# Performance work log

Measured on AMD Instinct MI355X. Metric: run time of the kernel, lower is better.

The kernel has to match this reference:

```python
import jax, jax.numpy as jnp
import numpy as np

B, N, C, H = 8, 1024, 1024, 16  # batch, seq, dim, heads
HID = 4 * C                     # mlp hidden (mlp_ratio=4.0)


def _ln(x, g, b, eps=1e-5):
    m = x.mean(-1, keepdims=True)
    v = ((x - m) ** 2).mean(-1, keepdims=True)
    return (x - m) / jnp.sqrt(v + eps) * g + b


def setup_inputs() -> dict:
    key = jax.random.key(0)
    ks = jax.random.split(key, 8)
    s = 0.02  # init scale
    f32 = jnp.float32
    return {
        "x": jax.random.normal(ks[0], (B, N, C), f32),
        "g1": jnp.ones((C,), f32), "b1": jnp.zeros((C,), f32),
        "Wq": jax.random.normal(ks[1], (C, C), f32) * s, "bq": jnp.zeros((C,), f32),
        "Wk": jax.random.normal(ks[2], (C, C), f32) * s, "bk": jnp.zeros((C,), f32),
        "Wv": jax.random.normal(ks[3], (C, C), f32) * s, "bv": jnp.zeros((C,), f32),
        "Wp": jax.random.normal(ks[4], (C, C), f32) * s, "bp": jnp.zeros((C,), f32),
        "g2": jnp.ones((C,), f32), "b2": jnp.zeros((C,), f32),
        "W1": jax.random.normal(ks[5], (C, HID), f32) * s, "c1": jnp.zeros((HID,), f32),
        "W2": jax.random.normal(ks[6], (HID, C), f32) * s, "c2": jnp.zeros((C,), f32),
    }


def reference(x, g1, b1, Wq, bq, Wk, bk, Wv, bv, Wp, bp, g2, b2, W1, c1, W2, c2):
    hd = C // H
    scale = hd ** -0.5
    # --- pre-norm self-attention ---
    h = _ln(x, g1, b1)
    # NOTE: faithful to source: direct reshape (B,N,C)->(B,H,N,hd), NOT the
    # standard reshape(B,N,H,hd).transpose -- the original code reshapes the
    # flat N*C block into H contiguous chunks of N*hd.
    q = (h @ Wq + bq).reshape(B, H, -1, hd)
    k = (h @ Wk + bk).reshape(B, H, -1, hd)
    v = (h @ Wv + bv).reshape(B, H, -1, hd)
    attn = jax.nn.softmax(jnp.einsum('bhnd,bhmd->bhnm', q, k) * scale, axis=-1)
    o = jnp.einsum('bhnm,bhmd->bhnd', attn, v)
    o = jnp.swapaxes(o, 1, 2).reshape(B, -1, C)  # (B,N,C)
    x = x + (o @ Wp + bp)
    # --- MLP block ---
    h2 = _ln(x, g2, b2)
    m = jax.nn.gelu(h2 @ W1 + c1, approximate=False) @ W2 + c2
    return x + m
```

## Files before the change

### kernel.cpp

```cpp
#include <hip/hip_runtime.h>
#include <hip/hip_bf16.h>
#include <math.h>

typedef __bf16 bf16_t;
typedef __bf16 bf16x4 __attribute__((ext_vector_type(4)));
typedef __bf16 bf16x8 __attribute__((ext_vector_type(8)));
typedef float  f32x4  __attribute__((ext_vector_type(4)));

typedef __attribute__((address_space(1))) const void GVoid;
typedef __attribute__((address_space(3))) void LVoid;

__device__ __forceinline__ void gld16(const void* g, void* l) {
    __builtin_amdgcn_global_load_lds((GVoid*)g, (LVoid*)l, 16, 0, 0);
}

__device__ __forceinline__ float gelu_exact(float v) {
    return 0.5f * v * (1.0f + erff(v * 0.7071067811865475f));
}

__global__ __launch_bounds__(256) void transpose_f32_bf16(
    const float* __restrict__ in, bf16_t* __restrict__ out,
    int R, int C, size_t inBatch, size_t outBatch)
{
    __shared__ bf16_t tile[64][65];
    const float* src = in  + (size_t)blockIdx.z * inBatch;
    bf16_t*      dst = out + (size_t)blockIdx.z * outBatch;
    const int r0 = blockIdx.y * 64, c0 = blockIdx.x * 64;
    const int t = threadIdx.x, tc = t & 63, tr = t >> 6;
#pragma unroll
    for (int i = 0; i < 16; ++i) {
        int r = tr + i * 4;
        tile[r][tc] = (bf16_t)src[(size_t)(r0 + r) * C + c0 + tc];
    }
    __syncthreads();
#pragma unroll
    for (int i = 0; i < 16; ++i) {
        int r = tr + i * 4;
        dst[(size_t)(c0 + r) * R + r0 + tc] = tile[tc][r];
    }
}

__global__ __launch_bounds__(256) void transpose_bf16(
    const bf16_t* __restrict__ in, bf16_t* __restrict__ out,
    int R, int C, size_t inBatch, size_t outBatch)
{
    __shared__ __align__(16) bf16_t tile[64][65];
    const bf16_t* src = in  + (size_t)blockIdx.z * inBatch;
    bf16_t*       dst = out + (size_t)blockIdx.z * outBatch;
    const int r0 = blockIdx.y * 64, c0 = blockIdx.x * 64;
    const int t = threadIdx.x, tc = t & 63, tr = t >> 6;
#pragma unroll
    for (int i = 0; i < 16; ++i) {
        int r = tr + i * 4;
        tile[r][tc] = src[(size_t)(r0 + r) * C + c0 + tc];
    }
    __syncthreads();
#pragma unroll
    for (int i = 0; i < 16; ++i) {
        int r = tr + i * 4;
        dst[(size_t)(c0 + r) * R + r0 + tc] = tile[tc][r];
    }
}

__global__ __launch_bounds__(256) void ln_kernel(
    const float* __restrict__ x, const float* __restrict__ g,
    const float* __restrict__ b, bf16_t* __restrict__ out)
{
    const int row = blockIdx.x, t = threadIdx.x;
    const float4 v4 = ((const float4*)(x + (size_t)row * 1024))[t];
    float v[4] = {v4.x, v4.y, v4.z, v4.w};
    float s = v[0] + v[1] + v[2] + v[3];
    float s2 = v[0]*v[0] + v[1]*v[1] + v[2]*v[2] + v[3]*v[3];
#pragma unroll
    for (int o = 1; o < 64; o <<= 1) { s += __shfl_xor(s, o); s2 += __shfl_xor(s2, o); }
    __shared__ float red[8];
    if ((t & 63) == 0) { red[t >> 6] = s; red[4 + (t >> 6)] = s2; }
    __syncthreads();
    s  = red[0] + red[1] + red[2] + red[3];
    s2 = red[4] + red[5] + red[6] + red[7];
    const float mean = s * (1.f / 1024.f);
    const float var  = fmaxf(s2 * (1.f / 1024.f) - mean * mean, 0.f);
    const float rstd = rsqrtf(var + 1e-5f);
    const float4 g4 = ((const float4*)g)[t];
    const float4 b4 = ((const float4*)b)[t];
    bf16x4 o;
    o[0] = (bf16_t)((v[0] - mean) * rstd * g4.x + b4.x);
    o[1] = (bf16_t)((v[1] - mean) * rstd * g4.y + b4.y);
    o[2] = (bf16_t)((v[2] - mean) * rstd * g4.z + b4.z);
    o[3] = (bf16_t)((v[3] - mean) * rstd * g4.w + b4.w);
    *(bf16x4*)(out + (size_t)row * 1024 + t * 4) = o;
}

__device__ __forceinline__ bf16x8 lds_rd(const char* base, int rl, int colB) {
    return *(const bf16x8*)(base + rl * 128 + (colB ^ ((rl & 7) << 4)));
}

template <int MODE>
__global__ __launch_bounds__(512, 2) void gemm256(
    const bf16_t* __restrict__ A, const bf16_t* __restrict__ Bt,
    const float* __restrict__ b0, const float* __restrict__ b1,
    const float* __restrict__ b2, const float* resid,
    bf16_t* __restrict__ ob0, bf16_t* __restrict__ ob1,
    bf16_t* __restrict__ ob2, float* of,
    int N, int K)
{
    __shared__ __align__(16) char lds[131072];
    const int t = threadIdx.x;
    const int w = t >> 6, ln = t & 63;
    const int wm = w >> 2, wn = w & 3;
    const int l16 = ln & 15, quad = ln >> 4;
    const int m0 = blockIdx.x * 256, n0 = blockIdx.y * 256;

    const bf16_t* gA = A  + (size_t)m0 * K;
    const bf16_t* gB = Bt + (size_t)n0 * K;

    const int w1k  = w << 10;
    const int srow = t >> 3;
    const int scol = ((t & 7) ^ (srow & 7)) << 3;

    auto stage = [&](int kt, int dbuf) {
        char* aL = (char*)lds + dbuf * 32768 + w1k;
        char* bL = (char*)lds + 65536 + dbuf * 32768 + w1k;
#pragma unroll
        for (int h = 0; h < 2; ++h) {
#pragma unroll
            for (int r2 = 0; r2 < 2; ++r2) {
                const int row = h * 128 + r2 * 64 + srow;
                gld16(gA + (size_t)row * K + kt + scol, aL + h * 16384 + r2 * 8192);
                gld16(gB + (size_t)row * K + kt + scol, bL + h * 16384 + r2 * 8192);
            }
        }
    };

    f32x4 acc[8][4];
#pragma unroll
    for (int i = 0; i < 8; ++i)
#pragma unroll
        for (int j = 0; j < 4; ++j) acc[i][j] = f32x4{0.f, 0.f, 0.f, 0.f};

    const int ktiles = K >> 6;
    stage(0, 0);
    stage(64, 1);
    asm volatile("s_waitcnt vmcnt(8)" ::: "memory");
    __builtin_amdgcn_s_barrier();
    __builtin_amdgcn_sched_barrier(0);

    bf16x8 af[4][2], bfr[4][2];

    for (int kt = 0; kt < ktiles; ++kt) {
        const int b = kt & 1;
        const char* aB = (const char*)lds + b * 32768 + wm * 16384;
        const char* bB = (const char*)lds + 65536 + b * 32768 + (wn >> 1) * 16384;
        const int bR0 = (wn & 1) << 6;

#pragma unroll
        for (int i = 0; i < 4; ++i)
#pragma unroll
            for (int ks = 0; ks < 2; ++ks)
                af[i][ks] = lds_rd(aB, i * 16 + l16, ks * 64 + quad * 16);
#pragma unroll
        for (int j = 0; j < 2; ++j)
#pragma unroll
            for (int ks = 0; ks < 2; ++ks)
                bfr[j][ks] = lds_rd(bB, bR0 + j * 16 + l16, ks * 64 + quad * 16);
        __builtin_amdgcn_s_setprio(1);
#pragma unroll
        for (int i = 0; i < 4; ++i)
#pragma unroll
            for (int j = 0; j < 2; ++j)
#pragma unroll
                for (int ks = 0; ks < 2; ++ks)
                    acc[i][j] = __builtin_amdgcn_mfma_f32_16x16x32_bf16(
                        af[i][ks], bfr[j][ks], acc[i][j], 0, 0, 0);
        __builtin_amdgcn_s_setprio(0);
        __builtin_amdgcn_sched_barrier(0);
        __builtin_amdgcn_s_barrier();

#pragma unroll
        for (int j = 2; j < 4; ++j)
#pragma unroll
            for (int ks = 0; ks < 2; ++ks)
                bfr[j][ks] = lds_rd(bB, bR0 + j * 16 + l16, ks * 64 + quad * 16);
        __builtin_amdgcn_s_setprio(1);
#pragma unroll
        for (int i = 0; i < 4; ++i)
#pragma unroll
            for (int j = 2; j < 4; ++j)
#pragma unroll
                for (int ks = 0; ks < 2; ++ks)
                    acc[i][j] = __builtin_amdgcn_mfma_f32_16x16x32_bf16(
                        af[i][ks], bfr[j][ks], acc[i][j], 0, 0, 0);
        __builtin_amdgcn_s_setprio(0);
        __builtin_amdgcn_sched_barrier(0);
        __builtin_amdgcn_s_barrier();

#pragma unroll
        for (int i = 0; i < 4; ++i)
#pragma unroll
            for (int ks = 0; ks < 2; ++ks)
                af[i][ks] = lds_rd(aB, 64 + i * 16 + l16, ks * 64 + quad * 16);
        __builtin_amdgcn_s_setprio(1);
#pragma unroll
        for (int i = 0; i < 4; ++i)
#pragma unroll
            for (int j = 2; j < 4; ++j)
#pragma unroll
                for (int ks = 0; ks < 2; ++ks)
                    acc[4 + i][j] = __builtin_amdgcn_mfma_f32_16x16x32_bf16(
                        af[i][ks], bfr[j][ks], acc[4 + i][j], 0, 0, 0);
        __builtin_amdgcn_s_setprio(0);
        __builtin_amdgcn_sched_barrier(0);
        asm volatile("s_waitcnt vmcnt(0)" ::: "memory");
        __builtin_amdgcn_s_barrier();
        __builtin_amdgcn_sched_barrier(0);

        if (kt + 2 < ktiles) stage((kt + 2) << 6, b);
        __builtin_amdgcn_s_setprio(1);
#pragma unroll
        for (int i = 0; i < 4; ++i)
#pragma unroll
            for (int j = 0; j < 2; ++j)
#pragma unroll
                for (int ks = 0; ks < 2; ++ks)
                    acc[4 + i][j] = __builtin_amdgcn_mfma_f32_16x16x32_bf16(
                        af[i][ks], bfr[j][ks], acc[4 + i][j], 0, 0, 0);
        __builtin_amdgcn_s_setprio(0);
        __builtin_amdgcn_sched_barrier(0);
    }

#pragma unroll
    for (int i = 0; i < 8; ++i) {
        const int rowb = m0 + wm * 128 + i * 16 + quad * 4;
#pragma unroll
        for (int j = 0; j < 4; ++j) {
            const int col = n0 + wn * 64 + j * 16 + l16;
            if (MODE == 0) {
                const int which = col >> 10;
                const float* bias = which == 0 ? b0 : (which == 1 ? b1 : b2);
                bf16_t* outp      = which == 0 ? ob0 : (which == 1 ? ob1 : ob2);
                const int cl = col & 1023;
                const float bc = bias[cl];
#pragma unroll
                for (int r = 0; r < 4; ++r)
                    outp[(size_t)(rowb + r) * 1024 + cl] = (bf16_t)(acc[i][j][r] + bc);
            } else if (MODE == 1) {
                const float bc = b0[col];
#pragma unroll
                for (int r = 0; r < 4; ++r) {
                    const size_t idx = (size_t)(rowb + r) * N + col;
                    of[idx] = acc[i][j][r] + bc + resid[idx];
                }
            } else if (MODE == 2) {
                const float bc = b0[col];
#pragma unroll
                for (int r = 0; r < 4; ++r)
                    ob0[(size_t)(rowb + r) * N + col] =
                        (bf16_t)gelu_exact(acc[i][j][r] + bc);
            } else {
#pragma unroll
                for (int r = 0; r < 4; ++r) {
                    const size_t idx = (size_t)(rowb + r) * N + col;
                    of[idx] += acc[i][j][r];
                }
            }
        }
    }
}

__global__ __launch_bounds__(256, 2) void attn_kernel(
    const bf16_t* __restrict__ Q, const bf16_t* __restrict__ K,
    const bf16_t* __restrict__ Vt, bf16_t* __restrict__ O)
{
    __shared__ __align__(16) bf16_t smem[26112];
    bf16_t* Vs = smem;
    bf16_t* Ks = smem + 8704;
    bf16_t* Ps = smem + 8704;

    const int t = threadIdx.x;
    const int wv = t >> 6, ln = t & 63;
    const int l16 = ln & 15, quad = ln >> 4;
    const int qt = blockIdx.x, bh = blockIdx.y;
    const size_t hb = (size_t)bh << 16;

    bf16x8 qf[2][2];
#pragma unroll
    for (int rt = 0; rt < 2; ++rt)
#pragma unroll
        for (int ks = 0; ks < 2; ++ks)
            qf[rt][ks] = *(const bf16x8*)(Q + hb +
                (size_t)(qt*128 + wv*32 + rt*16 + l16) * 64 + ks*32 + quad*8);

    float m_run[2] = {-INFINITY, -INFINITY};
    float l_run[2] = {0.f, 0.f};
    f32x4 acc_o[2][4];
#pragma unroll
    for (int rt = 0; rt < 2; ++rt)
#pragma unroll
        for (int dt = 0; dt < 4; ++dt) acc_o[rt][dt] = f32x4{0.f, 0.f, 0.f, 0.f};

    const int krow = t >> 3, kcol = (t & 7) << 3;
    const int vrow = t >> 4, vcol = (t & 15) << 3;
    const float sc = 0.125f;

    for (int j = 0; j < 8; ++j) {
        bf16x8 kg[4], vg[4];
#pragma unroll
        for (int i = 0; i < 4; ++i) {
            kg[i] = *(const bf16x8*)(K  + hb + (size_t)(j*128 + i*32 + krow)*64 + kcol);
            vg[i] = *(const bf16x8*)(Vt + hb + (size_t)(i*16 + vrow)*1024 + j*128 + vcol);
        }
        __syncthreads();
#pragma unroll
        for (int i = 0; i < 4; ++i) {
            *(bf16x8*)(Ks + (i*32 + krow)*72 + kcol)  = kg[i];
            *(bf16x8*)(Vs + (i*16 + vrow)*136 + vcol) = vg[i];
        }
        __syncthreads();

        f32x4 accs[8][2];
#pragma unroll
        for (int nt = 0; nt < 8; ++nt)
#pragma unroll
            for (int rt = 0; rt < 2; ++rt) accs[nt][rt] = f32x4{0.f, 0.f, 0.f, 0.f};
#pragma unroll
        for (int ks = 0; ks < 2; ++ks)
#pragma unroll
            for (int nt = 0; nt < 8; ++nt) {
                bf16x8 kf = *(const bf16x8*)(Ks + (nt*16 + l16)*72 + ks*32 + quad*8);
#pragma unroll
                for (int rt = 0; rt < 2; ++rt)
                    accs[nt][rt] = __builtin_amdgcn_mfma_f32_16x16x32_bf16(
                        kf, qf[rt][ks], accs[nt][rt], 0, 0, 0);
            }

#pragma unroll
        for (int rt = 0; rt < 2; ++rt) {
            float mx = -INFINITY;
#pragma unroll
            for (int nt = 0; nt < 8; ++nt)
#pragma unroll
                for (int r = 0; r < 4; ++r) mx = fmaxf(mx, accs[nt][rt][r]);
            mx *= sc;
            mx = fmaxf(mx, __shfl_xor(mx, 16));
            mx = fmaxf(mx, __shfl_xor(mx, 32));
            const float mnew  = fmaxf(m_run[rt], mx);
            const float alpha = __expf(m_run[rt] - mnew);
            m_run[rt] = mnew;
            float rs = 0.f;
#pragma unroll
            for (int nt = 0; nt < 8; ++nt)
#pragma unroll
                for (int r = 0; r < 4; ++r) {
                    float p = __expf(accs[nt][rt][r] * sc - mnew);
                    accs[nt][rt][r] = p;
                    rs += p;
                }
            rs += __shfl_xor(rs, 16);
            rs += __shfl_xor(rs, 32);
            l_run[rt] = l_run[rt] * alpha + rs;
#pragma unroll
            for (int r = 0; r < 4; ++r) {
                const float af = __shfl(alpha, quad*4 + r, 16);
#pragma unroll
                for (int dt = 0; dt < 4; ++dt) acc_o[rt][dt][r] *= af;
            }
        }

        __syncthreads();
#pragma unroll
        for (int rt = 0; rt < 2; ++rt) {
            const int mrow = wv*32 + rt*16 + l16;
#pragma unroll
            for (int nt = 0; nt < 8; ++nt) {
                bf16x4 pk;
#pragma unroll
                for (int r = 0; r < 4; ++r) pk[r] = (bf16_t)accs[nt][rt][r];
                *(bf16x4*)(Ps + mrow*136 + nt*16 + quad*4) = pk;
            }
        }
#pragma unroll
        for (int ks = 0; ks < 4; ++ks) {
            bf16x8 ap[2];
#pragma unroll
            for (int rt = 0; rt < 2; ++rt)
                ap[rt] = *(const bf16x8*)(Ps + (wv*32 + rt*16 + l16)*136 + ks*32 + quad*8);
#pragma unroll
            for (int dt = 0; dt < 4; ++dt) {
                bf16x8 bvv = *(const bf16x8*)(Vs + (dt*16 + l16)*136 + ks*32 + quad*8);
#pragma unroll
                for (int rt = 0; rt < 2; ++rt)
                    acc_o[rt][dt] = __builtin_amdgcn_mfma_f32_16x16x32_bf16(
                        ap[rt], bvv, acc_o[rt][dt], 0, 0, 0);
            }
        }
    }

    const int b = bh >> 4, h = bh & 15;
#pragma unroll
    for (int rt = 0; rt < 2; ++rt) {
#pragma unroll
        for (int r = 0; r < 4; ++r) {
            const float inv = 1.f / __shfl(l_run[rt], quad*4 + r, 16);
            const int m = qt*128 + wv*32 + rt*16 + quad*4 + r;
#pragma unroll
            for (int dt = 0; dt < 4; ++dt) {
                const int d = dt*16 + l16;
                O[((size_t)b*1024 + m)*1024 + h*64 + d] =
                    (bf16_t)(acc_o[rt][dt][r] * inv);
            }
        }
    }
}

extern "C" void kernel_launch(void* const* d_in, const int* in_sizes, int n_in,
                              void* d_out, int out_size, void* d_ws, size_t ws_size,
                              hipStream_t stream)
{
    (void)in_sizes; (void)n_in;
    const size_t MB = 1ull << 20;
    if (ws_size < 64 * MB) {
        hipMemsetAsync(d_out, 0, (size_t)out_size * sizeof(float), stream);
        return;
    }

    const float* x  = (const float*)d_in[0];
    const float* g1 = (const float*)d_in[1];
    const float* b1 = (const float*)d_in[2];
    const float* Wq = (const float*)d_in[3];
    const float* bq = (const float*)d_in[4];
    const float* Wk = (const float*)d_in[5];
    const float* bk = (const float*)d_in[6];
    const float* Wv = (const float*)d_in[7];
    const float* bv = (const float*)d_in[8];
    const float* Wp = (const float*)d_in[9];
    const float* bp = (const float*)d_in[10];
    const float* g2 = (const float*)d_in[11];
    const float* b2 = (const float*)d_in[12];
    const float* W1 = (const float*)d_in[13];
    const float* c1 = (const float*)d_in[14];
    const float* W2 = (const float*)d_in[15];
    const float* c2 = (const float*)d_in[16];

    char* ws = (char*)d_ws;
    bf16_t* Kb  = (bf16_t*)(ws);
    bf16_t* Vb  = (bf16_t*)(ws + 16 * MB);
    bf16_t* Cs  = (bf16_t*)(ws + 32 * MB);
    bf16_t* WqT = (bf16_t*)(ws + 48 * MB);
    bf16_t* WpT = (bf16_t*)(ws + 54 * MB);
    bf16_t* W1T = (bf16_t*)(ws + 56 * MB);
    bf16_t* W2T = (bf16_t*)(ws + 48 * MB);
    bf16_t* Qb  = (bf16_t*)d_out;
    bf16_t* Ob  = Vb;
    bf16_t* hid = Kb;
    bf16_t* h2  = Cs;
    float*  x2  = (float*)d_out;
    float*  outf = (float*)d_out;

    const dim3 blk(256);
    const dim3 blk5(512);

    transpose_f32_bf16<<<dim3(16, 16, 1), blk, 0, stream>>>(Wq, WqT,              1024, 1024, 0, 0);
    transpose_f32_bf16<<<dim3(16, 16, 1), blk, 0, stream>>>(Wk, WqT + 1024*1024,  1024, 1024, 0, 0);
    transpose_f32_bf16<<<dim3(16, 16, 1), blk, 0, stream>>>(Wv, WqT + 2*1024*1024, 1024, 1024, 0, 0);
    transpose_f32_bf16<<<dim3(16, 16, 1), blk, 0, stream>>>(Wp, WpT,              1024, 1024, 0, 0);
    transpose_f32_bf16<<<dim3(64, 16, 1), blk, 0, stream>>>(W1, W1T,              1024, 4096, 0, 0);

    ln_kernel<<<8192, blk, 0, stream>>>(x, g1, b1, Cs);

    gemm256<0><<<dim3(32, 12), blk5, 0, stream>>>(
        Cs, WqT, bq, bk, bv, nullptr, Qb, Kb, Vb, nullptr, 3072, 1024);

    transpose_bf16<<<dim3(1, 16, 128), blk, 0, stream>>>(Vb, Cs, 1024, 64, 65536, 65536);

    attn_kernel<<<dim3(8, 128), blk, 0, stream>>>(Qb, Kb, Cs, Ob);

    gemm256<1><<<dim3(32, 4), blk5, 0, stream>>>(
        Ob, WpT, bp, nullptr, nullptr, x, nullptr, nullptr, nullptr, x2, 1024, 1024);

    transpose_f32_bf16<<<dim3(16, 32, 2), blk, 0, stream>>>(
        W2, W2T, 2048, 1024, 2048*1024, 2048*1024);

    ln_kernel<<<8192, blk, 0, stream>>>(x2, g2, b2, h2);

    for (int c = 0; c < 2; ++c) {
        gemm256<2><<<dim3(32, 8), blk5, 0, stream>>>(
            h2, W1T + (size_t)c * 2048 * 1024, c1 + c * 2048,
            nullptr, nullptr, nullptr, hid, nullptr, nullptr, nullptr, 2048, 1024);
        if (c == 0)
            gemm256<1><<<dim3(32, 4), blk5, 0, stream>>>(
                hid, W2T, c2, nullptr, nullptr, outf,
                nullptr, nullptr, nullptr, outf, 1024, 2048);
        else
            gemm256<5><<<dim3(32, 4), blk5, 0, stream>>>(
                hid, W2T + (size_t)2048 * 1024, nullptr, nullptr, nullptr, nullptr,
                nullptr, nullptr, nullptr, outf, 1024, 2048);
    }
}
```

Measured before the change: 611.0 us.

## Template GEMM on N-tile width and split staging into finer pipelined half-tiles

The GEMM is templated on the N tile width, with BN=128 used for the QKV, projection and W2 GEMMs to double their grid size and improve CU fill. The global-to-LDS staging is split into separate A and B half-tile loads, issued between MFMA phases with graded vmcnt waits. This replaces the single full-stage load followed by a vmcnt(0) drain and aims to overlap memory with compute. The warp layout is also changed to interleave rows and columns. The risks are more barriers per K-tile and lower arithmetic intensity from the smaller tiles.

Measured after the change: 534.5 us. -12.5%, faster.

```diff
diff --git a/kernel.cpp b/kernel.cpp
--- a/kernel.cpp
+++ b/kernel.cpp
@@ -17,6 +17,13 @@
 __device__ __forceinline__ float gelu_exact(float v) {
     return 0.5f * v * (1.0f + erff(v * 0.7071067811865475f));
 }
+
+__device__ __forceinline__ f32x4 MF(bf16x8 a, bf16x8 b, f32x4 c) {
+    return __builtin_amdgcn_mfma_f32_16x16x32_bf16(a, b, c, 0, 0, 0);
+}
+
+#define VMCNT(n) asm volatile("s_waitcnt vmcnt(" #n ")" ::: "memory")
+#define FENCE()  asm volatile("" ::: "memory")
 
 __global__ __launch_bounds__(256) void transpose_f32_bf16(
     const float* __restrict__ in, bf16_t* __restrict__ out,
@@ -91,25 +98,26 @@
     *(bf16x4*)(out + (size_t)row * 1024 + t * 4) = o;
 }
 
-__device__ __forceinline__ bf16x8 lds_rd(const char* base, int rl, int colB) {
-    return *(const bf16x8*)(base + rl * 128 + (colB ^ ((rl & 7) << 4)));
-}
-
-template <int MODE>
+template <int MODE, int BN>
 __global__ __launch_bounds__(512, 2) void gemm256(
     const bf16_t* __restrict__ A, const bf16_t* __restrict__ Bt,
     const float* __restrict__ b0, const float* __restrict__ b1,
     const float* __restrict__ b2, const float* resid,
     bf16_t* __restrict__ ob0, bf16_t* __restrict__ ob1,
-    bf16_t* __restrict__ ob2, float* of,
-    int N, int K)
+    bf16_t* __restrict__ ob2, float* of, int N, int K)
 {
-    __shared__ __align__(16) char lds[131072];
+    constexpr int NJ   = BN / 64;
+    constexpr int JH   = NJ / 2;
+    constexpr int BUFB = BN * 128;
+    constexpr int HBB  = BN * 64;
+    __shared__ __align__(16) char lds[65536 + 2 * BUFB];
+    char* ldsB = lds + 65536;
+
     const int t = threadIdx.x;
     const int w = t >> 6, ln = t & 63;
-    const int wm = w >> 2, wn = w & 3;
+    const int wm = w & 1, wn = w >> 1;
     const int l16 = ln & 15, quad = ln >> 4;
-    const int m0 = blockIdx.x * 256, n0 = blockIdx.y * 256;
+    const int m0 = blockIdx.x * 256, n0 = blockIdx.y * BN;
 
     const bf16_t* gA = A  + (size_t)m0 * K;
     const bf16_t* gB = Bt + (size_t)n0 * K;
@@ -118,123 +126,139 @@
     const int srow = t >> 3;
     const int scol = ((t & 7) ^ (srow & 7)) << 3;
 
-    auto stage = [&](int kt, int dbuf) {
-        char* aL = (char*)lds + dbuf * 32768 + w1k;
-        char* bL = (char*)lds + 65536 + dbuf * 32768 + w1k;
-#pragma unroll
-        for (int h = 0; h < 2; ++h) {
-#pragma unroll
-            for (int r2 = 0; r2 < 2; ++r2) {
-                const int row = h * 128 + r2 * 64 + srow;
-                gld16(gA + (size_t)row * K + kt + scol, aL + h * 16384 + r2 * 8192);
-                gld16(gB + (size_t)row * K + kt + scol, bL + h * 16384 + r2 * 8192);
-            }
-        }
+    auto stageA = [&](int kt, int h) {
+        char* dst = lds + (kt & 1) * 32768 + h * 16384 + w1k;
+        const bf16_t* s0 = gA + (size_t)(h * 128 + srow) * K + (kt << 6) + scol;
+        gld16(s0, dst);
+        gld16(s0 + (size_t)64 * K, dst + 8192);
     };
-
-    f32x4 acc[8][4];
+    auto stageB = [&](int kt, int h) {
+        char* dst = ldsB + (kt & 1) * BUFB + h * HBB + w1k;
+        if constexpr (BN == 256) {
+            const bf16_t* s0 = gB + (size_t)(h * 128 + srow) * K + (kt << 6) + scol;
+            gld16(s0, dst);
+            gld16(s0 + (size_t)64 * K, dst + 8192);
+        } else {
+            const bf16_t* s0 = gB + (size_t)(h * 64 + srow) * K + (kt << 6) + scol;
+            gld16(s0, dst);
+        }
+    };
+
+    auto rdA = [&](int q, int i, int ks) -> bf16x8 {
+        const int r = (i & 3) * 32 + wm * 16 + l16;
+        const char* p = lds + q * 32768 + (i >> 2) * 16384 + r * 128
+                        + ((ks * 64 + quad * 16) ^ ((r & 7) << 4));
+        return *(const bf16x8*)p;
+    };
+    auto rdB = [&](int q, int j, int ks) -> bf16x8 {
+        int half, r;
+        if constexpr (BN == 256) { half = j >> 1; r = (j & 1) * 64 + wn * 16 + l16; }
+        else                     { half = j;      r = wn * 16 + l16; }
+        const char* p = ldsB + q * BUFB + half * HBB + r * 128
+                        + ((ks * 64 + quad * 16) ^ ((r & 7) << 4));
+        return *(const bf16x8*)p;
+    };
+
+    f32x4 acc[8][NJ];
 #pragma unroll
     for (int i = 0; i < 8; ++i)
 #pragma unroll
-        for (int j = 0; j < 4; ++j) acc[i][j] = f32x4{0.f, 0.f, 0.f, 0.f};
+        for (int j = 0; j < NJ; ++j) acc[i][j] = f32x4{0.f, 0.f, 0.f, 0.f};
 
     const int ktiles = K >> 6;
-    stage(0, 0);
-    stage(64, 1);
-    asm volatile("s_waitcnt vmcnt(8)" ::: "memory");
-    __builtin_amdgcn_s_barrier();
-    __builtin_amdgcn_sched_barrier(0);
-
-    bf16x8 af[4][2], bfr[4][2];
-
-    for (int kt = 0; kt < ktiles; ++kt) {
-        const int b = kt & 1;
-        const char* aB = (const char*)lds + b * 32768 + wm * 16384;
-        const char* bB = (const char*)lds + 65536 + b * 32768 + (wn >> 1) * 16384;
-        const int bR0 = (wn & 1) << 6;
-
+
+    stageA(0, 0); stageB(0, 0); stageA(0, 1); stageB(0, 1);
+    stageA(1, 0); stageB(1, 0); stageA(1, 1);
+
+    bf16x8 afr[4][2], bL[JH][2], bH[JH][2];
+
+    for (int T = 0; T < ktiles; ++T) {
+        const int q = T & 1;
+        const bool notlast = (T + 1 < ktiles);
+        const bool st2     = (T + 2 < ktiles);
+
+        if (notlast) { if constexpr (BN == 256) VMCNT(10); else VMCNT(8); }
+        else         { if constexpr (BN == 256) VMCNT(4);  else VMCNT(3); }
+        __builtin_amdgcn_s_barrier();
+        FENCE(); __builtin_amdgcn_sched_barrier(0);
+        if (notlast) stageB(T + 1, 1);
 #pragma unroll
         for (int i = 0; i < 4; ++i)
 #pragma unroll
-            for (int ks = 0; ks < 2; ++ks)
-                af[i][ks] = lds_rd(aB, i * 16 + l16, ks * 64 + quad * 16);
-#pragma unroll
-        for (int j = 0; j < 2; ++j)
-#pragma unroll
-            for (int ks = 0; ks < 2; ++ks)
-                bfr[j][ks] = lds_rd(bB, bR0 + j * 16 + l16, ks * 64 + quad * 16);
+            for (int ks = 0; ks < 2; ++ks) afr[i][ks] = rdA(q, i, ks);
+#pragma unroll
+        for (int j = 0; j < JH; ++j)
+#pragma unroll
+            for (int ks = 0; ks < 2; ++ks) bL[j][ks] = rdB(q, j, ks);
         __builtin_amdgcn_s_setprio(1);
 #pragma unroll
         for (int i = 0; i < 4; ++i)
 #pragma unroll
-            for (int j = 0; j < 2; ++j)
+            for (int j = 0; j < JH; ++j)
 #pragma unroll
                 for (int ks = 0; ks < 2; ++ks)
-                    acc[i][j] = __builtin_amdgcn_mfma_f32_16x16x32_bf16(
-                        af[i][ks], bfr[j][ks], acc[i][j], 0, 0, 0);
+                    acc[i][j] = MF(afr[i][ks], bL[j][ks], acc[i][j]);
         __builtin_amdgcn_s_setprio(0);
         __builtin_amdgcn_sched_barrier(0);
+
+        if (notlast) { if constexpr (BN == 256) VMCNT(8); else VMCNT(6); }
+        else         VMCNT(0);
         __builtin_amdgcn_s_barrier();
-
-#pragma unroll
-        for (int j = 2; j < 4; ++j)
-#pragma unroll
-            for (int ks = 0; ks < 2; ++ks)
-                bfr[j][ks] = lds_rd(bB, bR0 + j * 16 + l16, ks * 64 + quad * 16);
+        FENCE(); __builtin_amdgcn_sched_barrier(0);
+        if (st2) stageA(T + 2, 0);
+#pragma unroll
+        for (int j = 0; j < JH; ++j)
+#pragma unroll
+            for (int ks = 0; ks < 2; ++ks) bH[j][ks] = rdB(q, JH + j, ks);
         __builtin_amdgcn_s_setprio(1);
 #pragma unroll
         for (int i = 0; i < 4; ++i)
 #pragma unroll
-            for (int j = 2; j < 4; ++j)
+            for (int j = 0; j < JH; ++j)
 #pragma unroll
                 for (int ks = 0; ks < 2; ++ks)
-                    acc[i][j] = __builtin_amdgcn_mfma_f32_16x16x32_bf16(
-                        af[i][ks], bfr[j][ks], acc[i][j], 0, 0, 0);
+                    acc[i][JH + j] = MF(afr[i][ks], bH[j][ks], acc[i][JH + j]);
         __builtin_amdgcn_s_setprio(0);
         __builtin_amdgcn_sched_barrier(0);
-        __builtin_amdgcn_s_barrier();
-
+
+        if (st2) stageB(T + 2, 0);
 #pragma unroll
         for (int i = 0; i < 4; ++i)
 #pragma unroll
-            for (int ks = 0; ks < 2; ++ks)
-                af[i][ks] = lds_rd(aB, 64 + i * 16 + l16, ks * 64 + quad * 16);
+            for (int ks = 0; ks < 2; ++ks) afr[i][ks] = rdA(q, 4 + i, ks);
         __builtin_amdgcn_s_setprio(1);
 #pragma unroll
         for (int i = 0; i < 4; ++i)
 #pragma unroll
-            for (int j = 2; j < 4; ++j)
+            for (int j = 0; j < JH; ++j)
 #pragma unroll
                 for (int ks = 0; ks < 2; ++ks)
-                    acc[4 + i][j] = __builtin_amdgcn_mfma_f32_16x16x32_bf16(
-                        af[i][ks], bfr[j][ks], acc[4 + i][j], 0, 0, 0);
+                    acc[4 + i][JH + j] = MF(afr[i][ks], bH[j][ks], acc[4 + i][JH + j]);
         __builtin_amdgcn_s_setprio(0);
         __builtin_amdgcn_sched_barrier(0);
-        asm volatile("s_waitcnt vmcnt(0)" ::: "memory");
+
         __builtin_amdgcn_s_barrier();
-        __builtin_amdgcn_sched_barrier(0);
-
-        if (kt + 2 < ktiles) stage((kt + 2) << 6, b);
+        FENCE(); __builtin_amdgcn_sched_barrier(0);
+        if (st2) stageA(T + 2, 1);
         __builtin_amdgcn_s_setprio(1);
 #pragma unroll
         for (int i = 0; i < 4; ++i)
 #pragma unroll
-            for (int j = 0; j < 2; ++j)
+            for (int j = 0; j < JH; ++j)
 #pragma unroll
                 for (int ks = 0; ks < 2; ++ks)
-                    acc[4 + i][j] = __builtin_amdgcn_mfma_f32_16x16x32_bf16(
-                        af[i][ks], bfr[j][ks], acc[4 + i][j], 0, 0, 0);
+                    acc[4 + i][j] = MF(afr[i][ks], bL[j][ks], acc[4 + i][j]);
         __builtin_amdgcn_s_setprio(0);
         __builtin_amdgcn_sched_barrier(0);
     }
 
 #pragma unroll
     for (int i = 0; i < 8; ++i) {
-        const int rowb = m0 + wm * 128 + i * 16 + quad * 4;
-#pragma unroll
-        for (int j = 0; j < 4; ++j) {
-            const int col = n0 + wn * 64 + j * 16 + l16;
-            if (MODE == 0) {
+        const int rowb = m0 + i * 32 + wm * 16 + quad * 4;
+#pragma unroll
+        for (int j = 0; j < NJ; ++j) {
+            const int col = n0 + j * 64 + wn * 16 + l16;
+            if constexpr (MODE == 0) {
                 const int which = col >> 10;
                 const float* bias = which == 0 ? b0 : (which == 1 ? b1 : b2);
                 bf16_t* outp      = which == 0 ? ob0 : (which == 1 ? ob1 : ob2);
@@ -243,14 +267,14 @@
 #pragma unroll
                 for (int r = 0; r < 4; ++r)
                     outp[(size_t)(rowb + r) * 1024 + cl] = (bf16_t)(acc[i][j][r] + bc);
-            } else if (MODE == 1) {
+            } else if constexpr (MODE == 1) {
                 const float bc = b0[col];
 #pragma unroll
                 for (int r = 0; r < 4; ++r) {
                     const size_t idx = (size_t)(rowb + r) * N + col;
                     of[idx] = acc[i][j][r] + bc + resid[idx];
                 }
-            } else if (MODE == 2) {
+            } else if constexpr (MODE == 2) {
                 const float bc = b0[col];
 #pragma unroll
                 for (int r = 0; r < 4; ++r)
@@ -467,14 +491,14 @@
 
     ln_kernel<<<8192, blk, 0, stream>>>(x, g1, b1, Cs);
 
-    gemm256<0><<<dim3(32, 12), blk5, 0, stream>>>(
+    gemm256<0, 128><<<dim3(32, 24), blk5, 0, stream>>>(
         Cs, WqT, bq, bk, bv, nullptr, Qb, Kb, Vb, nullptr, 3072, 1024);
 
     transpose_bf16<<<dim3(1, 16, 128), blk, 0, stream>>>(Vb, Cs, 1024, 64, 65536, 65536);
 
     attn_kernel<<<dim3(8, 128), blk, 0, stream>>>(Qb, Kb, Cs, Ob);
 
-    gemm256<1><<<dim3(32, 4), blk5, 0, stream>>>(
+    gemm256<1, 128><<<dim3(32, 8), blk5, 0, stream>>>(
         Ob, WpT, bp, nullptr, nullptr, x, nullptr, nullptr, nullptr, x2, 1024, 1024);
 
     transpose_f32_bf16<<<dim3(16, 32, 2), blk, 0, stream>>>(
@@ -483,15 +507,15 @@
     ln_kernel<<<8192, blk, 0, stream>>>(x2, g2, b2, h2);
 
     for (int c = 0; c < 2; ++c) {
-        gemm256<2><<<dim3(32, 8), blk5, 0, stream>>>(
+        gemm256<2, 256><<<dim3(32, 8), blk5, 0, stream>>>(
             h2, W1T + (size_t)c * 2048 * 1024, c1 + c * 2048,
             nullptr, nullptr, nullptr, hid, nullptr, nullptr, nullptr, 2048, 1024);
         if (c == 0)
-            gemm256<1><<<dim3(32, 4), blk5, 0, stream>>>(
+            gemm256<1, 128><<<dim3(32, 8), blk5, 0, stream>>>(
                 hid, W2T, c2, nullptr, nullptr, outf,
                 nullptr, nullptr, nullptr, outf, 1024, 2048);
         else
-            gemm256<5><<<dim3(32, 4), blk5, 0, stream>>>(
+            gemm256<5, 128><<<dim3(32, 8), blk5, 0, stream>>>(
                 hid, W2T + (size_t)2048 * 1024, nullptr, nullptr, nullptr, nullptr,
                 nullptr, nullptr, nullptr, outf, 1024, 2048);
     }
```
